# Performance work log

Hardware: AMD Instinct MI355X
Metric: run time of the kernel (lower is better)

The kernel has to match this reference:

```python
import jax, jax.numpy as jnp
import numpy as np
from jax import lax

NUM_HEADS = 8
KERNEL_SIZE = 7
PADDING_L = 3
EPS = 1e-12


def pow2_quantize(w):
    # LinearShift: weights constrained to sign * 2^round(log2|w|) (bit-shift arithmetic),
    # with straight-through estimator for gradients.
    wq = jnp.sign(w) * jnp.exp2(jnp.round(jnp.log2(jnp.abs(w) + EPS)))
    return w + lax.stop_gradient(wq - w)


def setup_inputs() -> dict:
    key = jax.random.key(0)
    k1, k2, k3 = jax.random.split(key, 3)
    T, B, C = 4096, 16, 512
    x = jax.random.normal(k1, (T, B, C), dtype=jnp.float32)
    shift_W = jax.random.normal(k2, (C, C), dtype=jnp.float32) * (1.0 / np.sqrt(C))
    shift_b = jnp.zeros((C,), dtype=jnp.float32)
    # xavier-uniform-ish init for the light-conv weight (H, K)
    lim = np.sqrt(6.0 / (NUM_HEADS + KERNEL_SIZE))
    weight = jax.random.uniform(k3, (NUM_HEADS, KERNEL_SIZE), minval=-lim, maxval=lim, dtype=jnp.float32)
    return {"x": x, "shift_W": shift_W, "shift_b": shift_b, "weight": weight}


def reference(x, shift_W, shift_b, weight):
    T, B, C = x.shape
    H, K = weight.shape
    R = C // H
    # 1) shift-linear: power-of-two quantized weights, y = x @ Wq^T + b  (T,B,C)
    Wq = pow2_quantize(shift_W)
    y = jnp.einsum("tbc,dc->tbd", x, Wq) + shift_b
    # 2) light (depthwise, head-shared) convolution along time
    xc = jnp.transpose(y, (1, 2, 0))  # (B, C, T)
    w = jax.nn.softmax(weight, axis=-1)  # weight_softmax=True
    # expand head kernels to per-channel depthwise kernels: (C, 1, K)
    w_full = jnp.repeat(w, R, axis=0)[:, None, :]
    out = lax.conv_general_dilated(
        xc, w_full,
        window_strides=(1,),
        padding=[(PADDING_L, K - 1 - PADDING_L)],
        dimension_numbers=("NCH", "OIH", "NCH"),
        feature_group_count=C,
    )  # (B, C, T)
    return jnp.transpose(out, (2, 0, 1))  # (T, B, C)
```

## Files before the change

### kernel.cpp

```cpp
#include <hip/hip_runtime.h>

constexpr int T_DIM = 4096;
constexpr int B_DIM = 16;
constexpr int C_DIM = 512;
constexpr int K_CONV = 7;
constexpr int M_DIM = T_DIM * B_DIM;
constexpr int BC = B_DIM * C_DIM;

typedef __attribute__((ext_vector_type(8))) short bf16x8;
typedef __attribute__((ext_vector_type(4))) float f32x4;
typedef __attribute__((ext_vector_type(8))) float f32x8;
typedef __attribute__((ext_vector_type(4))) unsigned int u32x4;

__device__ __forceinline__ unsigned short f2bf(float f) {
  unsigned u = __float_as_uint(f);
  u += 0x7fffu + ((u >> 16) & 1u);
  return (unsigned short)(u >> 16);
}
__device__ __forceinline__ unsigned pack2(float a, float b) {
  return (unsigned)f2bf(a) | (((unsigned)f2bf(b)) << 16);
}
__device__ __forceinline__ u32x4 pack8(f32x4 lo, f32x4 hi) {
  u32x4 o;
  o[0] = pack2(lo[0], lo[1]);
  o[1] = pack2(lo[2], lo[3]);
  o[2] = pack2(hi[0], hi[1]);
  o[3] = pack2(hi[2], hi[3]);
  return o;
}

__global__ __launch_bounds__(256) void quantize_w(
    const float* __restrict__ W, unsigned short* __restrict__ Wq) {
  int i = blockIdx.x * 256 + threadIdx.x;
  float w = W[i];
  float a = fabsf(w) + 1e-12f;
  float q = exp2f(rintf(log2f(a)));
  q = (w > 0.f) ? q : ((w < 0.f) ? -q : 0.f);
  Wq[i] = f2bf(q);
}

constexpr int BK = 32;
constexpr int LDS_STRIDE = 40;

__global__ __launch_bounds__(256, 2) void gemm_bt(
    const float* __restrict__ X, const short* __restrict__ Bt,
    const float* __restrict__ bias, unsigned short* __restrict__ Y) {
  constexpr int K = C_DIM, N = C_DIM;
  __shared__ __align__(16) short As[128 * LDS_STRIDE];
  __shared__ __align__(16) short Bs[128 * LDS_STRIDE];

  const int id   = blockIdx.x;
  const int xcd  = id & 7;
  const int slot = id >> 3;
  const int nb   = slot & 3;
  const int mb   = xcd * 64 + (slot >> 2);
  const int m0 = mb * 128;
  const int n0 = nb * 128;

  const int t    = threadIdx.x;
  const int lane = t & 63;
  const int wid  = t >> 6;

  const int sr = t >> 2;
  const int sc = (t & 3) * 8;
  const float* pX0 = X + (long)(m0 + sr) * K + sc;
  const float* pX1 = X + (long)(m0 + 64 + sr) * K + sc;
  const short* pB0 = Bt + (long)(n0 + sr) * K + sc;
  const short* pB1 = Bt + (long)(n0 + 64 + sr) * K + sc;

  const int fr = lane & 15;
  const int fq = lane >> 4;
  const int wm = (wid >> 1) * 64;
  const int wn = (wid & 1) * 64;

  f32x4 acc[4][4] = {};

  f32x4 xa0 = *(const f32x4*)(pX0);
  f32x4 xa1 = *(const f32x4*)(pX0 + 4);
  f32x4 xb0 = *(const f32x4*)(pX1);
  f32x4 xb1 = *(const f32x4*)(pX1 + 4);
  bf16x8 b0 = *(const bf16x8*)(pB0);
  bf16x8 b1 = *(const bf16x8*)(pB1);

  for (int k0 = 0; k0 < K; k0 += BK) {
    u32x4 a0 = pack8(xa0, xa1);
    u32x4 a1 = pack8(xb0, xb1);
    bf16x8 bs0 = b0, bs1 = b1;
    __syncthreads();
    *(u32x4*)&As[sr * LDS_STRIDE + sc]         = a0;
    *(u32x4*)&As[(64 + sr) * LDS_STRIDE + sc]  = a1;
    *(bf16x8*)&Bs[sr * LDS_STRIDE + sc]        = bs0;
    *(bf16x8*)&Bs[(64 + sr) * LDS_STRIDE + sc] = bs1;
    __syncthreads();

    if (k0 + BK < K) {
      xa0 = *(const f32x4*)(pX0 + k0 + BK);
      xa1 = *(const f32x4*)(pX0 + k0 + BK + 4);
      xb0 = *(const f32x4*)(pX1 + k0 + BK);
      xb1 = *(const f32x4*)(pX1 + k0 + BK + 4);
      b0 = *(const bf16x8*)(pB0 + k0 + BK);
      b1 = *(const bf16x8*)(pB1 + k0 + BK);
    }

    bf16x8 af[4], bfr[4];
#pragma unroll
    for (int i = 0; i < 4; ++i)
      af[i] = *(const bf16x8*)&As[(wm + i * 16 + fr) * LDS_STRIDE + fq * 8];
#pragma unroll
    for (int j = 0; j < 4; ++j)
      bfr[j] = *(const bf16x8*)&Bs[(wn + j * 16 + fr) * LDS_STRIDE + fq * 8];
#pragma unroll
    for (int i = 0; i < 4; ++i)
#pragma unroll
      for (int j = 0; j < 4; ++j)
        acc[i][j] = __builtin_amdgcn_mfma_f32_16x16x32_bf16(af[i], bfr[j], acc[i][j], 0, 0, 0);
  }

#pragma unroll
  for (int j = 0; j < 4; ++j) {
    const int gn = n0 + wn + j * 16 + fr;
    const float bv = bias[gn];
#pragma unroll
    for (int i = 0; i < 4; ++i) {
#pragma unroll
      for (int r = 0; r < 4; ++r) {
        const int gm = m0 + wm + i * 16 + fq * 4 + r;
        Y[(long)gm * N + gn] = f2bf(acc[i][j][r] + bv);
      }
    }
  }
}

constexpr int CHT = 32;

__device__ __forceinline__ u32x4 loadY(const unsigned short* Y, int t, long off) {
  if ((unsigned)t < (unsigned)T_DIM)
    return *(const u32x4*)(Y + (long)t * BC + off);
  u32x4 z = {0u, 0u, 0u, 0u};
  return z;
}

__device__ __forceinline__ f32x8 unpack8(u32x4 u) {
  f32x8 r;
#pragma unroll
  for (int i = 0; i < 4; ++i) {
    unsigned w = u[i];
    r[2 * i]     = __uint_as_float(w << 16);
    r[2 * i + 1] = __uint_as_float(w & 0xffff0000u);
  }
  return r;
}

__global__ __launch_bounds__(256) void lconv(
    const unsigned short* __restrict__ Y, const float* __restrict__ W,
    float* __restrict__ O) {
  const int tid  = blockIdx.x * 256 + threadIdx.x;
  const int cvec = tid & 63;
  const int b    = (tid >> 6) & 15;
  const int tc   = tid >> 10;
  const int t0   = tc * CHT;
  const long off = (long)b * C_DIM + cvec * 8;
  const int h    = cvec >> 3;

  float wf[K_CONV];
  float mx = -1e30f;
#pragma unroll
  for (int k = 0; k < K_CONV; ++k) { wf[k] = W[h * K_CONV + k]; mx = fmaxf(mx, wf[k]); }
  float s = 0.f;
#pragma unroll
  for (int k = 0; k < K_CONV; ++k) { wf[k] = __expf(wf[k] - mx); s += wf[k]; }
  const float inv = 1.f / s;
#pragma unroll
  for (int k = 0; k < K_CONV; ++k) wf[k] *= inv;

  f32x8 win[K_CONV];
#pragma unroll
  for (int i = 0; i < 6; ++i) win[i] = unpack8(loadY(Y, t0 - 3 + i, off));

#pragma unroll
  for (int j = 0; j < CHT; ++j) {
    win[6] = unpack8(loadY(Y, t0 + 3 + j, off));
    f32x8 acc = win[0] * wf[0];
#pragma unroll
    for (int k = 1; k < K_CONV; ++k) acc += win[k] * wf[k];
    float* op = O + (long)(t0 + j) * BC + off;
    *(f32x4*)op       = f32x4{acc[0], acc[1], acc[2], acc[3]};
    *(f32x4*)(op + 4) = f32x4{acc[4], acc[5], acc[6], acc[7]};
#pragma unroll
    for (int k = 0; k < 6; ++k) win[k] = win[k + 1];
  }
}

extern "C" void kernel_launch(void* const* d_in, const int* in_sizes, int n_in,
                              void* d_out, int out_size, void* d_ws, size_t ws_size,
                              hipStream_t stream) {
  const float* x       = (const float*)d_in[0];
  const float* shift_W = (const float*)d_in[1];
  const float* shift_b = (const float*)d_in[2];
  const float* weight  = (const float*)d_in[3];
  float* out = (float*)d_out;

  unsigned short* Wq = (unsigned short*)d_ws;
  unsigned short* Y  = Wq + C_DIM * C_DIM;

  quantize_w<<<(C_DIM * C_DIM) / 256, 256, 0, stream>>>(shift_W, Wq);
  gemm_bt<<<(M_DIM / 128) * (C_DIM / 128), 256, 0, stream>>>(
      x, (const short*)Wq, shift_b, Y);
  lconv<<<(M_DIM / CHT) * (C_DIM / 8) / 256, 256, 0, stream>>>(Y, weight, out);
}
```

Before: 320.6 us.

## Double-buffer GEMM LDS with BK=64, XOR swizzle, and async B loads

Restructures the shift-linear GEMM main loop. It doubles BK to 64, double-buffers the A and B tiles in LDS with a single barrier per step, and replaces padded rows with an XOR-swizzled layout. B is now staged straight into LDS via global_load_lds. The goal is to hide global load latency behind MFMA work and cut barrier and bank-conflict overhead, at the cost of more LDS and registers that could limit occupancy. It also halves the light-conv time chunk to launch more threads.

New measurement: 324.4 us. About the same (+1.2%).

```diff
diff --git a/kernel.cpp b/kernel.cpp
--- a/kernel.cpp
+++ b/kernel.cpp
@@ -11,6 +11,7 @@
 typedef __attribute__((ext_vector_type(4))) float f32x4;
 typedef __attribute__((ext_vector_type(8))) float f32x8;
 typedef __attribute__((ext_vector_type(4))) unsigned int u32x4;
+typedef __attribute__((ext_vector_type(2))) unsigned int u32x2;
 
 __device__ __forceinline__ unsigned short f2bf(float f) {
   unsigned u = __float_as_uint(f);
@@ -19,14 +20,6 @@
 }
 __device__ __forceinline__ unsigned pack2(float a, float b) {
   return (unsigned)f2bf(a) | (((unsigned)f2bf(b)) << 16);
-}
-__device__ __forceinline__ u32x4 pack8(f32x4 lo, f32x4 hi) {
-  u32x4 o;
-  o[0] = pack2(lo[0], lo[1]);
-  o[1] = pack2(lo[2], lo[3]);
-  o[2] = pack2(hi[0], hi[1]);
-  o[3] = pack2(hi[2], hi[3]);
-  return o;
 }
 
 __global__ __launch_bounds__(256) void quantize_w(
@@ -39,15 +32,15 @@
   Wq[i] = f2bf(q);
 }
 
-constexpr int BK = 32;
-constexpr int LDS_STRIDE = 40;
+constexpr int BK = 64;
+constexpr int NSTEP = C_DIM / BK;
 
 __global__ __launch_bounds__(256, 2) void gemm_bt(
     const float* __restrict__ X, const short* __restrict__ Bt,
     const float* __restrict__ bias, unsigned short* __restrict__ Y) {
   constexpr int K = C_DIM, N = C_DIM;
-  __shared__ __align__(16) short As[128 * LDS_STRIDE];
-  __shared__ __align__(16) short Bs[128 * LDS_STRIDE];
+  __shared__ __align__(16) short As[2][128 * BK];
+  __shared__ __align__(16) short Bs[2][128 * BK];
 
   const int id   = blockIdx.x;
   const int xcd  = id & 7;
@@ -61,59 +54,86 @@
   const int lane = t & 63;
   const int wid  = t >> 6;
 
-  const int sr = t >> 2;
-  const int sc = (t & 3) * 8;
-  const float* pX0 = X + (long)(m0 + sr) * K + sc;
-  const float* pX1 = X + (long)(m0 + 64 + sr) * K + sc;
-  const short* pB0 = Bt + (long)(n0 + sr) * K + sc;
-  const short* pB1 = Bt + (long)(n0 + 64 + sr) * K + sc;
+  const int arow = t >> 4;
+  const int acol = (t & 15) * 4;
+  const float* pA = X + (long)(m0 + arow) * K + acol;
+  const int awoff = ((((acol >> 3) ^ (arow & 7)) << 4) | ((acol & 4) << 1));
+
+  const int brow = (wid << 5) + (lane >> 3);
+  const int bcol = ((lane & 7) ^ ((lane >> 3) & 7)) * 8;
+  const short* pB = Bt + (long)(n0 + brow) * K + bcol;
 
   const int fr = lane & 15;
   const int fq = lane >> 4;
   const int wm = (wid >> 1) * 64;
   const int wn = (wid & 1) * 64;
-
+  const int sw0 = ((fq ^ (fr & 7)) << 4);
+  const int sw1 = (((4 + fq) ^ (fr & 7)) << 4);
+
+  f32x4 ax[8];
   f32x4 acc[4][4] = {};
 
-  f32x4 xa0 = *(const f32x4*)(pX0);
-  f32x4 xa1 = *(const f32x4*)(pX0 + 4);
-  f32x4 xb0 = *(const f32x4*)(pX1);
-  f32x4 xb1 = *(const f32x4*)(pX1 + 4);
-  bf16x8 b0 = *(const bf16x8*)(pB0);
-  bf16x8 b1 = *(const bf16x8*)(pB1);
-
-  for (int k0 = 0; k0 < K; k0 += BK) {
-    u32x4 a0 = pack8(xa0, xa1);
-    u32x4 a1 = pack8(xb0, xb1);
-    bf16x8 bs0 = b0, bs1 = b1;
-    __syncthreads();
-    *(u32x4*)&As[sr * LDS_STRIDE + sc]         = a0;
-    *(u32x4*)&As[(64 + sr) * LDS_STRIDE + sc]  = a1;
-    *(bf16x8*)&Bs[sr * LDS_STRIDE + sc]        = bs0;
-    *(bf16x8*)&Bs[(64 + sr) * LDS_STRIDE + sc] = bs1;
-    __syncthreads();
-
-    if (k0 + BK < K) {
-      xa0 = *(const f32x4*)(pX0 + k0 + BK);
-      xa1 = *(const f32x4*)(pX0 + k0 + BK + 4);
-      xb0 = *(const f32x4*)(pX1 + k0 + BK);
-      xb1 = *(const f32x4*)(pX1 + k0 + BK + 4);
-      b0 = *(const bf16x8*)(pB0 + k0 + BK);
-      b1 = *(const bf16x8*)(pB1 + k0 + BK);
-    }
-
-    bf16x8 af[4], bfr[4];
+  auto loadA = [&](int k0) {
+#pragma unroll
+    for (int j = 0; j < 8; ++j)
+      ax[j] = *(const f32x4*)(pA + (long)j * 16 * K + k0);
+  };
+  auto stageB = [&](int bsel, int k0) {
 #pragma unroll
     for (int i = 0; i < 4; ++i)
-      af[i] = *(const bf16x8*)&As[(wm + i * 16 + fr) * LDS_STRIDE + fq * 8];
-#pragma unroll
-    for (int j = 0; j < 4; ++j)
-      bfr[j] = *(const bf16x8*)&Bs[(wn + j * 16 + fr) * LDS_STRIDE + fq * 8];
-#pragma unroll
-    for (int i = 0; i < 4; ++i)
+      __builtin_amdgcn_global_load_lds(
+          (const __attribute__((address_space(1))) void*)(pB + (long)i * 8 * K + k0),
+          (__attribute__((address_space(3))) void*)&Bs[bsel][wid * 2048 + i * 512],
+          16, 0, 0);
+  };
+  auto writeA = [&](int bsel) {
+    char* base = (char*)&As[bsel][0];
+#pragma unroll
+    for (int j = 0; j < 8; ++j) {
+      u32x2 p;
+      p[0] = pack2(ax[j][0], ax[j][1]);
+      p[1] = pack2(ax[j][2], ax[j][3]);
+      *(u32x2*)(base + (j * 16 + arow) * 128 + awoff) = p;
+    }
+  };
+  auto compute = [&](int bsel) {
+    const char* ab = (const char*)&As[bsel][0];
+    const char* bb = (const char*)&Bs[bsel][0];
+#pragma unroll
+    for (int kk = 0; kk < 2; ++kk) {
+      const int sw = kk ? sw1 : sw0;
+      bf16x8 af[4], bfr[4];
+#pragma unroll
+      for (int i = 0; i < 4; ++i)
+        af[i] = *(const bf16x8*)(ab + (wm + i * 16 + fr) * 128 + sw);
 #pragma unroll
       for (int j = 0; j < 4; ++j)
-        acc[i][j] = __builtin_amdgcn_mfma_f32_16x16x32_bf16(af[i], bfr[j], acc[i][j], 0, 0, 0);
+        bfr[j] = *(const bf16x8*)(bb + (wn + j * 16 + fr) * 128 + sw);
+#pragma unroll
+      for (int i = 0; i < 4; ++i)
+#pragma unroll
+        for (int j = 0; j < 4; ++j)
+          acc[i][j] = __builtin_amdgcn_mfma_f32_16x16x32_bf16(af[i], bfr[j], acc[i][j], 0, 0, 0);
+    }
+  };
+
+  loadA(0);
+  stageB(0, 0);
+  writeA(0);
+  __syncthreads();
+
+#pragma unroll
+  for (int s = 0; s < NSTEP; ++s) {
+    const int buf = s & 1;
+    if (s + 1 < NSTEP) {
+      loadA((s + 1) * BK);
+      stageB(buf ^ 1, (s + 1) * BK);
+    }
+    compute(buf);
+    if (s + 1 < NSTEP) {
+      writeA(buf ^ 1);
+      __syncthreads();
+    }
   }
 
 #pragma unroll
@@ -131,7 +151,7 @@
   }
 }
 
-constexpr int CHT = 32;
+constexpr int CHT = 16;
 
 __device__ __forceinline__ u32x4 loadY(const unsigned short* Y, int t, long off) {
   if ((unsigned)t < (unsigned)T_DIM)
```
